# Kernel optimization log

Measured on AMD Instinct MI355X. Metric: run time of the kernel, lower is better.

## Reference

```python
import jax, jax.numpy as jnp
import numpy as np

IN_C, HID1, HID2 = 128, 256, 32
N_NODES = 50000
N_EDGES = 1600000
N_LABEL = 200000


def setup_inputs() -> dict:
    key = jax.random.key(0)
    ks = jax.random.split(key, 8)
    x = jax.random.normal(ks[0], (N_NODES, IN_C), dtype=jnp.float32)
    edge_index = jax.random.randint(ks[1], (2, N_EDGES), 0, N_NODES, dtype=jnp.int64)
    edge_label_index = jax.random.randint(ks[2], (2, N_LABEL), 0, N_NODES, dtype=jnp.int64)
    # GCNConv params (glorot-ish scale), bias zeros as default init
    W1 = jax.random.normal(ks[3], (IN_C, HID1), dtype=jnp.float32) * (1.0 / np.sqrt(IN_C))
    b1 = jnp.zeros((HID1,), dtype=jnp.float32)
    W2 = jax.random.normal(ks[4], (HID1, HID2), dtype=jnp.float32) * (1.0 / np.sqrt(HID1))
    b2 = jnp.zeros((HID2,), dtype=jnp.float32)
    return {"x": x, "edge_index": edge_index, "edge_label_index": edge_label_index,
            "W1": W1, "b1": b1, "W2": W2, "b2": b2}


def _gcn_conv(x, W, b, src, dst, n_nodes):
    # GCNConv: h = x @ W; add self-loops; symmetric deg^{-1/2} normalization; scatter-add; + bias
    h = x @ W  # [N, out]
    loop = jnp.arange(n_nodes, dtype=src.dtype)
    s = jnp.concatenate([src, loop])
    d = jnp.concatenate([dst, loop])
    deg = jax.ops.segment_sum(jnp.ones_like(d, dtype=h.dtype), d, num_segments=n_nodes)
    dinv = jnp.where(deg > 0, jax.lax.rsqrt(deg), 0.0)
    coef = dinv[s] * dinv[d]  # [E+N]
    msg = h[s] * coef[:, None]  # irregular gather, [E+N, out]
    agg = jax.ops.segment_sum(msg, d, num_segments=n_nodes)
    return agg + b


def reference(x, edge_index, edge_label_index, W1, b1, W2, b2):
    n = x.shape[0]
    src, dst = edge_index[0], edge_index[1]
    # encode (dropout p=0, use_bn=False -> identity)
    h = _gcn_conv(x, W1, b1, src, dst, n)
    h = jax.nn.relu(h)
    z = _gcn_conv(h, W2, b2, src, dst, n)
    # decode: edge-wise dot product
    return (z[edge_label_index[0]] * z[edge_label_index[1]]).sum(axis=-1)
```

## Files before the change

### kernel.cpp

```cpp
#include <hip/hip_runtime.h>
#include <hip/hip_fp16.h>

#define IN_C 128
#define H1   256
#define H2   32
#define BWL  6
#define NBMAX 1024

typedef _Float16 half8 __attribute__((ext_vector_type(8)));
typedef _Float16 half4 __attribute__((ext_vector_type(4)));
typedef _Float16 h2    __attribute__((ext_vector_type(2)));
typedef float f32x4 __attribute__((ext_vector_type(4)));

__global__ __launch_bounds__(256) void k_cast(const float4* __restrict__ x4, const float* __restrict__ dinv,
                                              h2* __restrict__ xh, int n4) {
  int i = blockIdx.x * 256 + threadIdx.x;
  if (i < n4) {
    float4 v = x4[i];
    float dn = dinv[i >> 5];
    h2 a, b;
    a[0] = (_Float16)(v.x * dn); a[1] = (_Float16)(v.y * dn);
    b[0] = (_Float16)(v.z * dn); b[1] = (_Float16)(v.w * dn);
    xh[2 * i] = a; xh[2 * i + 1] = b;
  }
}

__global__ __launch_bounds__(256) void k_castw(const float* __restrict__ W1, const float* __restrict__ W2,
                                               _Float16* __restrict__ W1s, _Float16* __restrict__ W2s,
                                               int* bucket_cnt, int* bucket_cursor, int nb) {
  int i = blockIdx.x * 256 + threadIdx.x;
  if (i < 128 * 256) {
    int d = i >> 3, j = i & 7;
    int mrow = d & 15, quad = (d >> 4) & 3, ks = (d >> 6) & 3, nt = d >> 8;
    W1s[i] = (_Float16)W1[(ks * 32 + quad * 8 + j) * 256 + nt * 16 + mrow];
  }
  if (i < 32 * 256) {
    int d = i >> 3, j = i & 7;
    int mrow = d & 15, quad = (d >> 4) & 3, ks = (d >> 6) & 7, nt = d >> 9;
    W2s[i] = (_Float16)W2[(ks * 32 + quad * 8 + j) * 32 + nt * 16 + mrow];
  }
  if (i <= nb) { bucket_cnt[i] = 0; bucket_cursor[i] = 0; }
}

__global__ __launch_bounds__(256) void k_bin(const int* __restrict__ dst, int* bucket_cnt, int e, int nb) {
  __shared__ int hist[NBMAX];
  for (int u = threadIdx.x; u < nb; u += 256) hist[u] = 0;
  __syncthreads();
  int base = blockIdx.x * 2048;
  #pragma unroll
  for (int j = 0; j < 8; j++) {
    int i = base + j * 256 + threadIdx.x;
    if (i < e) atomicAdd(&hist[dst[i] >> BWL], 1);
  }
  __syncthreads();
  for (int u = threadIdx.x; u < nb; u += 256) if (hist[u]) atomicAdd(&bucket_cnt[u], hist[u]);
}

__global__ __launch_bounds__(256) void k_scan_bkt(const int* __restrict__ bucket_cnt,
                                                  int* __restrict__ bucket_base, int nb) {
  __shared__ int tsum[256];
  int t = threadIdx.x;
  int v[4]; int s = 0;
  #pragma unroll
  for (int k = 0; k < 4; k++) {
    int idx = t * 4 + k;
    int c = (idx < nb) ? bucket_cnt[idx] : 0;
    v[k] = s; s += c;
  }
  tsum[t] = s; __syncthreads();
  for (int off = 1; off < 256; off <<= 1) {
    int x = (t >= off) ? tsum[t - off] : 0;
    __syncthreads();
    tsum[t] += x;
    __syncthreads();
  }
  int excl = tsum[t] - s;
  #pragma unroll
  for (int k = 0; k < 4; k++) {
    int idx = t * 4 + k;
    if (idx < nb) bucket_base[idx] = excl + v[k];
  }
  if (t == 255) bucket_base[nb] = tsum[255];
}

__global__ __launch_bounds__(256) void k_scatter(const int* __restrict__ src, const int* __restrict__ dst,
                                                 const int* __restrict__ bucket_base, int* bucket_cursor,
                                                 unsigned int* __restrict__ binned, int e, int nb) {
  __shared__ int hist[NBMAX];
  __shared__ int wbase[NBMAX];
  int t = threadIdx.x;
  for (int u = t; u < nb; u += 256) hist[u] = 0;
  __syncthreads();
  int base = blockIdx.x * 4096;
  int s_[16], d_[16];
  #pragma unroll
  for (int j = 0; j < 16; j++) {
    int i = base + j * 256 + t;
    if (i < e) {
      s_[j] = src[i]; d_[j] = dst[i];
      atomicAdd(&hist[d_[j] >> BWL], 1);
    } else d_[j] = -1;
  }
  __syncthreads();
  for (int u = t; u < nb; u += 256) {
    int c = hist[u];
    wbase[u] = (c > 0) ? (bucket_base[u] + atomicAdd(&bucket_cursor[u], c)) : 0;
  }
  __syncthreads();
  for (int u = t; u < nb; u += 256) hist[u] = 0;
  __syncthreads();
  #pragma unroll
  for (int j = 0; j < 16; j++) {
    if (d_[j] >= 0) {
      int b = d_[j] >> BWL;
      int r = atomicAdd(&hist[b], 1);
      binned[wbase[b] + r] = ((unsigned)(d_[j] & 63) << 16) | (unsigned)s_[j];
    }
  }
}

__global__ __launch_bounds__(256) void k_fill2(const unsigned int* __restrict__ binned,
                                               const int* __restrict__ bucket_base,
                                               int* __restrict__ csr_src,
                                               int* __restrict__ offsets, int* __restrict__ ecnt,
                                               float* __restrict__ dinv, int n, int nb) {
  __shared__ int cnt[64], pre[64], cur[64], loc[64];
  int b = blockIdx.x;
  int t = threadIdx.x;
  if (t < 64) { cnt[t] = 0; cur[t] = 0; }
  __syncthreads();
  int start = bucket_base[b], end = bucket_base[b + 1];
  int node0 = b << BWL;
  for (int i = start + t; i < end; i += 256) {
    int li = (int)(binned[i] >> 16);
    atomicAdd(&cnt[li], 1);
  }
  __syncthreads();
  int v = (t < 64) ? cnt[t] : 0;
  if (t < 64) pre[t] = v;
  __syncthreads();
  for (int off = 1; off < 64; off <<= 1) {
    int x = (t >= off && t < 64) ? pre[t - off] : 0;
    __syncthreads();
    if (t < 64) pre[t] += x;
    __syncthreads();
  }
  if (t < 64) {
    int excl = pre[t] - v;
    loc[t] = excl;
    int node = node0 + t;
    if (node < n) {
      offsets[node] = start + excl;
      ecnt[node] = v;
      dinv[node] = rsqrtf((float)(v + 1));
    }
  }
  __syncthreads();
  for (int i = start + t; i < end; i += 256) {
    unsigned int rec = binned[i];
    int li = (int)(rec >> 16);
    int p = atomicAdd(&cur[li], 1);
    csr_src[start + loc[li] + p] = (int)(rec & 0xFFFFu);
  }
}

__global__ __launch_bounds__(256) void k_agg1(const half8* __restrict__ xh8, const float* __restrict__ dinv,
                                              const int* __restrict__ ecnt, const int* __restrict__ offsets,
                                              const int* __restrict__ csr_src,
                                              half8* __restrict__ aggh8, int n) {
  int node = blockIdx.x * 4 + (threadIdx.x >> 6);
  int lane = threadIdx.x & 63;
  int g = lane >> 4;
  int c8 = lane & 15;
  if (node >= n) return;
  float acc[8];
  #pragma unroll
  for (int k = 0; k < 8; k++) acc[k] = 0.f;
  int start = offsets[node];
  int cnt = ecnt[node];
  int j = 0;
  for (; j + 32 <= cnt; j += 32) {
    int s0 = csr_src[start + j + g],      s1 = csr_src[start + j + 4 + g];
    int s2 = csr_src[start + j + 8 + g],  s3 = csr_src[start + j + 12 + g];
    int s4 = csr_src[start + j + 16 + g], s5 = csr_src[start + j + 20 + g];
    int s6 = csr_src[start + j + 24 + g], s7 = csr_src[start + j + 28 + g];
    half8 v0 = xh8[(size_t)s0 * 16 + c8], v1 = xh8[(size_t)s1 * 16 + c8];
    half8 v2 = xh8[(size_t)s2 * 16 + c8], v3 = xh8[(size_t)s3 * 16 + c8];
    half8 v4 = xh8[(size_t)s4 * 16 + c8], v5 = xh8[(size_t)s5 * 16 + c8];
    half8 v6 = xh8[(size_t)s6 * 16 + c8], v7 = xh8[(size_t)s7 * 16 + c8];
    half8 s = (((v0 + v1) + (v2 + v3)) + ((v4 + v5) + (v6 + v7)));
    #pragma unroll
    for (int k = 0; k < 8; k++) acc[k] += (float)s[k];
  }
  if (j + 16 <= cnt) {
    int s0 = csr_src[start + j + g],     s1 = csr_src[start + j + 4 + g];
    int s2 = csr_src[start + j + 8 + g], s3 = csr_src[start + j + 12 + g];
    half8 v0 = xh8[(size_t)s0 * 16 + c8], v1 = xh8[(size_t)s1 * 16 + c8];
    half8 v2 = xh8[(size_t)s2 * 16 + c8], v3 = xh8[(size_t)s3 * 16 + c8];
    half8 s = (v0 + v1) + (v2 + v3);
    #pragma unroll
    for (int k = 0; k < 8; k++) acc[k] += (float)s[k];
    j += 16;
  }
  for (int t = j + g; t < cnt; t += 4) {
    half8 v = xh8[(size_t)csr_src[start + t] * 16 + c8];
    #pragma unroll
    for (int k = 0; k < 8; k++) acc[k] += (float)v[k];
  }
  #pragma unroll
  for (int k = 0; k < 8; k++) {
    acc[k] += __shfl_xor(acc[k], 16, 64);
    acc[k] += __shfl_xor(acc[k], 32, 64);
  }
  if (g == 0) {
    half8 selfv = xh8[(size_t)node * 16 + c8];
    float dn = dinv[node];
    half8 o;
    #pragma unroll
    for (int k = 0; k < 8; k++) o[k] = (_Float16)((acc[k] + (float)selfv[k]) * dn);
    aggh8[(size_t)node * 16 + c8] = o;
  }
}

__global__ __launch_bounds__(256) void k_gemm1(const _Float16* __restrict__ aggh,
                                               const _Float16* __restrict__ W1s, const float* __restrict__ b1,
                                               _Float16* __restrict__ h1h, int n) {
  int wid = threadIdx.x >> 6, lane = threadIdx.x & 63;
  int quad = lane >> 4, mrow = lane & 15;
  int mbase = blockIdx.x * 64 + wid * 16;
  int node = mbase + mrow; if (node >= n) node = n - 1;
  const half8* A = (const half8*)aggh;
  const half8* B = (const half8*)W1s;
  f32x4 acc[16];
  #pragma unroll
  for (int t = 0; t < 16; t++) acc[t] = (f32x4){0.f, 0.f, 0.f, 0.f};
  half8 a_cur = A[(size_t)node * 16 + quad];
  #pragma unroll
  for (int ks = 0; ks < 4; ks++) {
    half8 bf[16];
    #pragma unroll
    for (int nt = 0; nt < 16; nt++) bf[nt] = B[(nt * 4 + ks) * 64 + lane];
    half8 a = a_cur;
    if (ks < 3) a_cur = A[(size_t)node * 16 + (ks + 1) * 4 + quad];
    #pragma unroll
    for (int nt = 0; nt < 16; nt++)
      acc[nt] = __builtin_amdgcn_mfma_f32_16x16x32_f16(a, bf[nt], acc[nt], 0, 0, 0);
  }
  #pragma unroll
  for (int nt = 0; nt < 16; nt++) {
    int c = nt * 16 + mrow;
    float bias = b1[c];
    #pragma unroll
    for (int r = 0; r < 4; r++) {
      int m = mbase + quad * 4 + r;
      if (m < n) h1h[(size_t)m * H1 + c] = (_Float16)fmaxf(acc[nt][r] + bias, 0.f);
    }
  }
}

__global__ __launch_bounds__(256) void k_gemm2(const _Float16* __restrict__ h1h,
                                               const _Float16* __restrict__ W2s, const float* __restrict__ dinv,
                                               _Float16* __restrict__ h2h, int n) {
  int wid = threadIdx.x >> 6, lane = threadIdx.x & 63;
  int quad = lane >> 4, mrow = lane & 15;
  int mbase = blockIdx.x * 64 + wid * 16;
  int node = mbase + mrow; if (node >= n) node = n - 1;
  const half8* A = (const half8*)h1h;
  const half8* B = (const half8*)W2s;
  f32x4 acc[2];
  acc[0] = (f32x4){0.f, 0.f, 0.f, 0.f};
  acc[1] = (f32x4){0.f, 0.f, 0.f, 0.f};
  half8 bf[16];
  #pragma unroll
  for (int ks = 0; ks < 8; ks++) {
    bf[2 * ks]     = B[(0 * 8 + ks) * 64 + lane];
    bf[2 * ks + 1] = B[(1 * 8 + ks) * 64 + lane];
  }
  half8 a_cur = A[(size_t)node * 32 + quad];
  #pragma unroll
  for (int ks = 0; ks < 8; ks++) {
    half8 a = a_cur;
    if (ks < 7) a_cur = A[(size_t)node * 32 + (ks + 1) * 4 + quad];
    acc[0] = __builtin_amdgcn_mfma_f32_16x16x32_f16(a, bf[2 * ks],     acc[0], 0, 0, 0);
    acc[1] = __builtin_amdgcn_mfma_f32_16x16x32_f16(a, bf[2 * ks + 1], acc[1], 0, 0, 0);
  }
  #pragma unroll
  for (int nt = 0; nt < 2; nt++) {
    int c = nt * 16 + mrow;
    #pragma unroll
    for (int r = 0; r < 4; r++) {
      int m = mbase + quad * 4 + r;
      if (m < n) h2h[(size_t)m * H2 + c] = (_Float16)(acc[nt][r] * dinv[m]);
    }
  }
}

__global__ __launch_bounds__(256) void k_agg2(const half4* __restrict__ h2h4, const float* __restrict__ dinv,
                                              const int* __restrict__ ecnt, const int* __restrict__ offsets,
                                              const int* __restrict__ csr_src,
                                              const float* __restrict__ b2, half4* __restrict__ zh4, int n) {
  int node = blockIdx.x * 4 + (threadIdx.x >> 6);
  int lane = threadIdx.x & 63;
  int g = lane >> 3;
  int c4 = lane & 7;
  if (node >= n) return;
  float acc[4];
  #pragma unroll
  for (int k = 0; k < 4; k++) acc[k] = 0.f;
  int start = offsets[node];
  int cnt = ecnt[node];
  int j = 0;
  for (; j + 32 <= cnt; j += 32) {
    int sA = csr_src[start + j + g],      sB = csr_src[start + j + 8 + g];
    int sC = csr_src[start + j + 16 + g], sD = csr_src[start + j + 24 + g];
    half4 vA = h2h4[(size_t)sA * 8 + c4], vB = h2h4[(size_t)sB * 8 + c4];
    half4 vC = h2h4[(size_t)sC * 8 + c4], vD = h2h4[(size_t)sD * 8 + c4];
    half4 s = (vA + vB) + (vC + vD);
    #pragma unroll
    for (int k = 0; k < 4; k++) acc[k] += (float)s[k];
  }
  if (j + 16 <= cnt) {
    int sA = csr_src[start + j + g], sB = csr_src[start + j + 8 + g];
    half4 s = h2h4[(size_t)sA * 8 + c4] + h2h4[(size_t)sB * 8 + c4];
    #pragma unroll
    for (int k = 0; k < 4; k++) acc[k] += (float)s[k];
    j += 16;
  }
  for (int t = j + g; t < cnt; t += 8) {
    half4 v = h2h4[(size_t)csr_src[start + t] * 8 + c4];
    #pragma unroll
    for (int k = 0; k < 4; k++) acc[k] += (float)v[k];
  }
  #pragma unroll
  for (int k = 0; k < 4; k++) {
    acc[k] += __shfl_xor(acc[k], 8, 64);
    acc[k] += __shfl_xor(acc[k], 16, 64);
    acc[k] += __shfl_xor(acc[k], 32, 64);
  }
  if (g == 0) {
    half4 selfv = h2h4[(size_t)node * 8 + c4];
    float dn = dinv[node];
    half4 o;
    #pragma unroll
    for (int k = 0; k < 4; k++) o[k] = (_Float16)((acc[k] + (float)selfv[k]) * dn + b2[c4 * 4 + k]);
    zh4[(size_t)node * 8 + c4] = o;
  }
}

__global__ __launch_bounds__(256) void k_decode(const half4* __restrict__ zh4, const int* __restrict__ eli,
                                                float* __restrict__ out, int L) {
  int p = blockIdx.x * 32 + (threadIdx.x >> 3);
  int c4 = threadIdx.x & 7;
  if (p >= L) return;
  int a = eli[p], b = eli[L + p];
  half4 za = zh4[(size_t)a * 8 + c4];
  half4 zb = zh4[(size_t)b * 8 + c4];
  h2 zal = {za[0], za[1]}, zah = {za[2], za[3]};
  h2 zbl = {zb[0], zb[1]}, zbh = {zb[2], zb[3]};
  float v = __builtin_amdgcn_fdot2(zal, zbl, __builtin_amdgcn_fdot2(zah, zbh, 0.f, false), false);
  #pragma unroll
  for (int off = 4; off >= 1; off >>= 1) v += __shfl_xor(v, off, 64);
  if (c4 == 0) out[p] = v;
}

extern "C" void kernel_launch(void* const* d_in, const int* in_sizes, int n_in,
                              void* d_out, int out_size, void* d_ws, size_t ws_size,
                              hipStream_t stream) {
  const float* x   = (const float*)d_in[0];
  const int*   ei  = (const int*)d_in[1];
  const int*   eli = (const int*)d_in[2];
  const float* W1  = (const float*)d_in[3];
  const float* b1  = (const float*)d_in[4];
  const float* W2  = (const float*)d_in[5];
  const float* b2  = (const float*)d_in[6];
  float* out = (float*)d_out;

  const int N = in_sizes[0] / IN_C;
  const int E = in_sizes[1] / 2;
  const int L = in_sizes[2] / 2;
  const int* e_src = ei;
  const int* e_dst = ei + E;
  const int NB = (N + 63) >> BWL;

  char* p = (char*)d_ws;
  auto carve = [&](size_t bytes) -> void* {
    void* r = (void*)p;
    p += (bytes + 255) & ~(size_t)255;
    return r;
  };
  int*   ecnt      = (int*)  carve((size_t)N * 4);
  float* dinv      = (float*)carve((size_t)N * 4);
  int*   offsets   = (int*)  carve((size_t)N * 4);
  int*   bcnt      = (int*)  carve((NBMAX + 1) * 4);
  int*   bbase     = (int*)  carve((NBMAX + 1) * 4);
  int*   bcursor   = (int*)  carve((NBMAX + 1) * 4);
  _Float16* W1s    = (_Float16*)carve(256 * 128 * 2);
  _Float16* W2s    = (_Float16*)carve(32 * 256 * 2);
  int*   csr_src   = (int*)  carve((size_t)E * 4);
  h2*    xh        = (h2*)   carve((size_t)N * IN_C * 2);
  h2*    aggh      = (h2*)   carve(((size_t)N + 64) * IN_C * 2);
  __half* h1h      = (__half*)carve(((size_t)N + 64) * H1 * 2);
  unsigned int* binned = (unsigned int*)h1h;
  _Float16* h2h = (_Float16*)aggh;
  half4* h2h4 = (half4*)aggh;
  half4* zh4  = (half4*)((char*)aggh + (size_t)N * H2 * 2);

  const int B = 256;
  k_castw<<<128, B, 0, stream>>>(W1, W2, W1s, W2s, bcnt, bcursor, NB);
  k_bin<<<(E + 2047) / 2048, B, 0, stream>>>(e_dst, bcnt, E, NB);
  k_scan_bkt<<<1, B, 0, stream>>>(bcnt, bbase, NB);
  k_scatter<<<(E + 4095) / 4096, B, 0, stream>>>(e_src, e_dst, bbase, bcursor, binned, E, NB);
  k_fill2<<<NB, B, 0, stream>>>(binned, bbase, csr_src, offsets, ecnt, dinv, N, NB);
  k_cast<<<(N * IN_C / 4 + B - 1) / B, B, 0, stream>>>((const float4*)x, dinv, xh, N * IN_C / 4);
  k_agg1<<<(N + 3) / 4, B, 0, stream>>>((const half8*)xh, dinv, ecnt, offsets, csr_src, (half8*)aggh, N);
  k_gemm1<<<(N + 63) / 64, B, 0, stream>>>((const _Float16*)aggh, W1s, b1, (_Float16*)h1h, N);
  k_gemm2<<<(N + 63) / 64, B, 0, stream>>>((const _Float16*)h1h, W2s, dinv, h2h, N);
  k_agg2<<<(N + 3) / 4, B, 0, stream>>>(h2h4, dinv, ecnt, offsets, csr_src, b2, zh4, N);
  k_decode<<<(L + 31) / 32, B, 0, stream>>>(zh4, eli, out, L);
}
```

Measured before the change: 262.6 us.

## Split layer-1 aggregation into four feature planes and use 16-bit CSR indices

```diff
diff --git a/kernel.cpp b/kernel.cpp
--- a/kernel.cpp
+++ b/kernel.cpp
@@ -13,15 +13,18 @@
 typedef float f32x4 __attribute__((ext_vector_type(4)));
 
 __global__ __launch_bounds__(256) void k_cast(const float4* __restrict__ x4, const float* __restrict__ dinv,
-                                              h2* __restrict__ xh, int n4) {
+                                              half4* __restrict__ xhp4, int n4, int n) {
   int i = blockIdx.x * 256 + threadIdx.x;
   if (i < n4) {
     float4 v = x4[i];
-    float dn = dinv[i >> 5];
-    h2 a, b;
-    a[0] = (_Float16)(v.x * dn); a[1] = (_Float16)(v.y * dn);
-    b[0] = (_Float16)(v.z * dn); b[1] = (_Float16)(v.w * dn);
-    xh[2 * i] = a; xh[2 * i + 1] = b;
+    int nd = i >> 5;
+    int p = (i & 31) >> 3;
+    int c4 = i & 7;
+    float dn = dinv[nd];
+    half4 o;
+    o[0] = (_Float16)(v.x * dn); o[1] = (_Float16)(v.y * dn);
+    o[2] = (_Float16)(v.z * dn); o[3] = (_Float16)(v.w * dn);
+    xhp4[((size_t)p * n + nd) * 8 + c4] = o;
   }
 }
 
@@ -121,7 +124,7 @@
 
 __global__ __launch_bounds__(256) void k_fill2(const unsigned int* __restrict__ binned,
                                                const int* __restrict__ bucket_base,
-                                               int* __restrict__ csr_src,
+                                               unsigned short* __restrict__ csr16,
                                                int* __restrict__ offsets, int* __restrict__ ecnt,
                                                float* __restrict__ dinv, int n, int nb) {
   __shared__ int cnt[64], pre[64], cur[64], loc[64];
@@ -160,19 +163,20 @@
     unsigned int rec = binned[i];
     int li = (int)(rec >> 16);
     int p = atomicAdd(&cur[li], 1);
-    csr_src[start + loc[li] + p] = (int)(rec & 0xFFFFu);
-  }
-}
-
-__global__ __launch_bounds__(256) void k_agg1(const half8* __restrict__ xh8, const float* __restrict__ dinv,
-                                              const int* __restrict__ ecnt, const int* __restrict__ offsets,
-                                              const int* __restrict__ csr_src,
-                                              half8* __restrict__ aggh8, int n) {
+    csr16[start + loc[li] + p] = (unsigned short)(rec & 0xFFFFu);
+  }
+}
+
+__global__ __launch_bounds__(256) void k_agg1p(const half8* __restrict__ xp8, const float* __restrict__ dinv,
+                                               const int* __restrict__ ecnt, const int* __restrict__ offsets,
+                                               const unsigned short* __restrict__ csr16,
+                                               half8* __restrict__ aggh8, int n, int plane) {
   int node = blockIdx.x * 4 + (threadIdx.x >> 6);
   int lane = threadIdx.x & 63;
-  int g = lane >> 4;
-  int c8 = lane & 15;
+  int grp = lane >> 2;
+  int c8 = lane & 3;
   if (node >= n) return;
+  const half8* xp = xp8 + (size_t)plane * n * 4;
   float acc[8];
   #pragma unroll
   for (int k = 0; k < 8; k++) acc[k] = 0.f;
@@ -180,45 +184,41 @@
   int cnt = ecnt[node];
   int j = 0;
   for (; j + 32 <= cnt; j += 32) {
-    int s0 = csr_src[start + j + g],      s1 = csr_src[start + j + 4 + g];
-    int s2 = csr_src[start + j + 8 + g],  s3 = csr_src[start + j + 12 + g];
-    int s4 = csr_src[start + j + 16 + g], s5 = csr_src[start + j + 20 + g];
-    int s6 = csr_src[start + j + 24 + g], s7 = csr_src[start + j + 28 + g];
-    half8 v0 = xh8[(size_t)s0 * 16 + c8], v1 = xh8[(size_t)s1 * 16 + c8];
-    half8 v2 = xh8[(size_t)s2 * 16 + c8], v3 = xh8[(size_t)s3 * 16 + c8];
-    half8 v4 = xh8[(size_t)s4 * 16 + c8], v5 = xh8[(size_t)s5 * 16 + c8];
-    half8 v6 = xh8[(size_t)s6 * 16 + c8], v7 = xh8[(size_t)s7 * 16 + c8];
-    half8 s = (((v0 + v1) + (v2 + v3)) + ((v4 + v5) + (v6 + v7)));
+    int sA = csr16[start + j + grp];
+    int sB = csr16[start + j + 16 + grp];
+    half8 vA = xp[(size_t)sA * 4 + c8];
+    half8 vB = xp[(size_t)sB * 4 + c8];
+    half8 s = vA + vB;
     #pragma unroll
     for (int k = 0; k < 8; k++) acc[k] += (float)s[k];
   }
   if (j + 16 <= cnt) {
-    int s0 = csr_src[start + j + g],     s1 = csr_src[start + j + 4 + g];
-    int s2 = csr_src[start + j + 8 + g], s3 = csr_src[start + j + 12 + g];
-    half8 v0 = xh8[(size_t)s0 * 16 + c8], v1 = xh8[(size_t)s1 * 16 + c8];
-    half8 v2 = xh8[(size_t)s2 * 16 + c8], v3 = xh8[(size_t)s3 * 16 + c8];
-    half8 s = (v0 + v1) + (v2 + v3);
-    #pragma unroll
-    for (int k = 0; k < 8; k++) acc[k] += (float)s[k];
+    int sA = csr16[start + j + grp];
+    half8 vA = xp[(size_t)sA * 4 + c8];
+    #pragma unroll
+    for (int k = 0; k < 8; k++) acc[k] += (float)vA[k];
     j += 16;
   }
-  for (int t = j + g; t < cnt; t += 4) {
-    half8 v = xh8[(size_t)csr_src[start + t] * 16 + c8];
-    #pragma unroll
-    for (int k = 0; k < 8; k++) acc[k] += (float)v[k];
+  if (j + grp < cnt) {
+    int sA = csr16[start + j + grp];
+    half8 vA = xp[(size_t)sA * 4 + c8];
+    #pragma unroll
+    for (int k = 0; k < 8; k++) acc[k] += (float)vA[k];
   }
   #pragma unroll
   for (int k = 0; k < 8; k++) {
+    acc[k] += __shfl_xor(acc[k], 4, 64);
+    acc[k] += __shfl_xor(acc[k], 8, 64);
     acc[k] += __shfl_xor(acc[k], 16, 64);
     acc[k] += __shfl_xor(acc[k], 32, 64);
   }
-  if (g == 0) {
-    half8 selfv = xh8[(size_t)node * 16 + c8];
+  if (grp == 0) {
+    half8 selfv = xp[(size_t)node * 4 + c8];
     float dn = dinv[node];
     half8 o;
     #pragma unroll
     for (int k = 0; k < 8; k++) o[k] = (_Float16)((acc[k] + (float)selfv[k]) * dn);
-    aggh8[(size_t)node * 16 + c8] = o;
+    aggh8[(size_t)node * 16 + plane * 4 + c8] = o;
   }
 }
 
@@ -297,7 +297,7 @@
 
 __global__ __launch_bounds__(256) void k_agg2(const half4* __restrict__ h2h4, const float* __restrict__ dinv,
                                               const int* __restrict__ ecnt, const int* __restrict__ offsets,
-                                              const int* __restrict__ csr_src,
+                                              const unsigned short* __restrict__ csr16,
                                               const float* __restrict__ b2, half4* __restrict__ zh4, int n) {
   int node = blockIdx.x * 4 + (threadIdx.x >> 6);
   int lane = threadIdx.x & 63;
@@ -311,8 +311,8 @@
   int cnt = ecnt[node];
   int j = 0;
   for (; j + 32 <= cnt; j += 32) {
-    int sA = csr_src[start + j + g],      sB = csr_src[start + j + 8 + g];
-    int sC = csr_src[start + j + 16 + g], sD = csr_src[start + j + 24 + g];
+    int sA = csr16[start + j + g],      sB = csr16[start + j + 8 + g];
+    int sC = csr16[start + j + 16 + g], sD = csr16[start + j + 24 + g];
     half4 vA = h2h4[(size_t)sA * 8 + c4], vB = h2h4[(size_t)sB * 8 + c4];
     half4 vC = h2h4[(size_t)sC * 8 + c4], vD = h2h4[(size_t)sD * 8 + c4];
     half4 s = (vA + vB) + (vC + vD);
@@ -320,14 +320,14 @@
     for (int k = 0; k < 4; k++) acc[k] += (float)s[k];
   }
   if (j + 16 <= cnt) {
-    int sA = csr_src[start + j + g], sB = csr_src[start + j + 8 + g];
+    int sA = csr16[start + j + g], sB = csr16[start + j + 8 + g];
     half4 s = h2h4[(size_t)sA * 8 + c4] + h2h4[(size_t)sB * 8 + c4];
     #pragma unroll
     for (int k = 0; k < 4; k++) acc[k] += (float)s[k];
     j += 16;
   }
   for (int t = j + g; t < cnt; t += 8) {
-    half4 v = h2h4[(size_t)csr_src[start + t] * 8 + c4];
+    half4 v = h2h4[(size_t)csr16[start + t] * 8 + c4];
     #pragma unroll
     for (int k = 0; k < 4; k++) acc[k] += (float)v[k];
   }
@@ -396,7 +396,7 @@
   int*   bcursor   = (int*)  carve((NBMAX + 1) * 4);
   _Float16* W1s    = (_Float16*)carve(256 * 128 * 2);
   _Float16* W2s    = (_Float16*)carve(32 * 256 * 2);
-  int*   csr_src   = (int*)  carve((size_t)E * 4);
+  unsigned short* csr16 = (unsigned short*)carve((size_t)E * 2);
   h2*    xh        = (h2*)   carve((size_t)N * IN_C * 2);
   h2*    aggh      = (h2*)   carve(((size_t)N + 64) * IN_C * 2);
   __half* h1h      = (__half*)carve(((size_t)N + 64) * H1 * 2);
@@ -410,11 +410,13 @@
   k_bin<<<(E + 2047) / 2048, B, 0, stream>>>(e_dst, bcnt, E, NB);
   k_scan_bkt<<<1, B, 0, stream>>>(bcnt, bbase, NB);
   k_scatter<<<(E + 4095) / 4096, B, 0, stream>>>(e_src, e_dst, bbase, bcursor, binned, E, NB);
-  k_fill2<<<NB, B, 0, stream>>>(binned, bbase, csr_src, offsets, ecnt, dinv, N, NB);
-  k_cast<<<(N * IN_C / 4 + B - 1) / B, B, 0, stream>>>((const float4*)x, dinv, xh, N * IN_C / 4);
-  k_agg1<<<(N + 3) / 4, B, 0, stream>>>((const half8*)xh, dinv, ecnt, offsets, csr_src, (half8*)aggh, N);
+  k_fill2<<<NB, B, 0, stream>>>(binned, bbase, csr16, offsets, ecnt, dinv, N, NB);
+  k_cast<<<(N * IN_C / 4 + B - 1) / B, B, 0, stream>>>((const float4*)x, dinv, (half4*)xh, N * IN_C / 4, N);
+  for (int plane = 0; plane < 4; plane++)
+    k_agg1p<<<(N + 3) / 4, B, 0, stream>>>((const half8*)xh, dinv, ecnt, offsets, csr16,
+                                           (half8*)aggh, N, plane);
   k_gemm1<<<(N + 63) / 64, B, 0, stream>>>((const _Float16*)aggh, W1s, b1, (_Float16*)h1h, N);
   k_gemm2<<<(N + 63) / 64, B, 0, stream>>>((const _Float16*)h1h, W2s, dinv, h2h, N);
-  k_agg2<<<(N + 3) / 4, B, 0, stream>>>(h2h4, dinv, ecnt, offsets, csr_src, b2, zh4, N);
+  k_agg2<<<(N + 3) / 4, B, 0, stream>>>(h2h4, dinv, ecnt, offsets, csr16, b2, zh4, N);
   k_decode<<<(L + 31) / 32, B, 0, stream>>>(zh4, eli, out, L);
 }
```

Measured after the change: 303.9 us. +15.7%, slower.
